# Kernel tuning notes

Measured on AMD Instinct MI355X. Metric: run time of the kernel, lower is better.

The kernel has to match this reference:

```python
import jax, jax.numpy as jnp
import numpy as np

B, T, H, V, L_IN, MAXLEN = 256, 128, 1024, 64, 457, 64


def setup_inputs() -> dict:
    key = jax.random.key(0)
    ks = jax.random.split(key, 12)
    s = 1.0 / np.sqrt(H)  # torch RNN default init scale
    w = lambda k, shape: jax.random.uniform(k, shape, jnp.float32, -s, s)
    z = jnp.zeros((H,), jnp.float32)
    return {
        "x": jax.random.normal(ks[0], (B, T, L_IN), dtype=jnp.float32),
        "emb": w(ks[1], (V, H)),
        # encoder RNN (tanh), 2 layers; b = b_ih + b_hh (mathematically identical)
        "enc_Wih0": w(ks[2], (H, L_IN)), "enc_Whh0": w(ks[3], (H, H)), "enc_b0": z,
        "enc_Wih1": w(ks[4], (H, H)),    "enc_Whh1": w(ks[5], (H, H)), "enc_b1": z,
        # decoder RNN (tanh), 2 layers
        "dec_Wih0": w(ks[6], (H, H)), "dec_Whh0": w(ks[7], (H, H)), "dec_b0": z,
        "dec_Wih1": w(ks[8], (H, H)), "dec_Whh1": w(ks[9], (H, H)), "dec_b1": z,
        "fc_W": w(ks[10], (V, H)), "fc_b": jnp.zeros((V,), jnp.float32),
    }


def _rnn_layer(xs, h0, Wih, Whh, b):
    # xs: [T, B, in]; h_t = tanh(x_t Wih^T + h_{t-1} Whh^T + b)
    def step(h, x_t):
        h = jnp.tanh(x_t @ Wih.T + h @ Whh.T + b)
        return h, h
    h_last, hs = jax.lax.scan(step, h0, xs)
    return hs, h_last


def reference(x, emb, enc_Wih0, enc_Whh0, enc_b0, enc_Wih1, enc_Whh1, enc_b1,
              dec_Wih0, dec_Whh0, dec_b0, dec_Wih1, dec_Whh1, dec_b1, fc_W, fc_b):
    Bc = x.shape[0]
    Hc = enc_Whh0.shape[0]
    xs = jnp.transpose(x, (1, 0, 2))  # [T, B, 457]
    h_init = jnp.zeros((Bc, Hc), x.dtype)
    # encoder: stacked 2-layer vanilla RNN
    hs0, hL0 = _rnn_layer(xs, h_init, enc_Wih0, enc_Whh0, enc_b0)
    hs1, hL1 = _rnn_layer(hs0, h_init, enc_Wih1, enc_Whh1, enc_b1)
    tok0 = jnp.zeros((Bc,), jnp.int32)

    def dec_step(carry, _):
        h0c, h1c, tok = carry
        e = emb[tok]                                        # [B, H]
        h0n = jnp.tanh(e @ dec_Wih0.T + h0c @ dec_Whh0.T + dec_b0)
        h1n = jnp.tanh(h0n @ dec_Wih1.T + h1c @ dec_Whh1.T + dec_b1)
        logits = h1n @ fc_W.T + fc_b                        # [B, V]
        nxt = jnp.argmax(logits, axis=-1).astype(jnp.int32)
        return (h0n, h1n, nxt), logits

    (hd0, hd1, _), logits_seq = jax.lax.scan(dec_step, (hL0, hL1, tok0), None, length=MAXLEN)
    vec_out = jnp.transpose(logits_seq, (1, 2, 0))          # [B, V, maxlen]
    hidden = jnp.stack([hd0, hd1], axis=0)                  # [n_layers, B, H]
    return vec_out, hidden
```

## Files before the change

kernel.cpp:

```cpp
#include <hip/hip_runtime.h>
#include <math.h>


#define Bb   256
#define Tt   128
#define Hh   1024
#define Vv   64
#define LIN  457
#define ML   64
#define NKB_H  32
#define NKB_X  15
#define XST  496

typedef __bf16 bf16;
typedef __bf16 bf16x8 __attribute__((ext_vector_type(8)));
typedef float  f32x4  __attribute__((ext_vector_type(4)));

static __device__ __forceinline__ float bf2f(bf16 x) {
    unsigned short u = __builtin_bit_cast(unsigned short, x);
    unsigned int w = ((unsigned int)u) << 16;
    return __builtin_bit_cast(float, w);
}
static __device__ __forceinline__ unsigned short f2bfbits(float f) {
    unsigned int u = __builtin_bit_cast(unsigned int, f);
    u = u + 0x7FFFu + ((u >> 16) & 1u);
    return (unsigned short)(u >> 16);
}
static __device__ __forceinline__ bf16 f2bf(float f) {
    return __builtin_bit_cast(bf16, f2bfbits(f));
}

#define MFMA(a, b, c) __builtin_amdgcn_mfma_f32_16x16x32_bf16((a), (b), (c), 0, 0, 0)

__global__ __launch_bounds__(256) void pack_w_k(const float* __restrict__ src,
                                                bf16* __restrict__ hp,
                                                bf16* __restrict__ lp,
                                                int nkb, int src_ld, int kmax) {
    const int tid = blockIdx.x * 256 + threadIdx.x;
    const int lane = tid & 63;
    const int kb = (tid >> 6) % nkb;
    const int nt = tid / (64 * nkb);
    if (nt >= 64) return;
    const int row = nt * 16 + (lane & 15);
    const int k0 = kb * 32 + (lane >> 4) * 8;
    const float* s = src + (size_t)row * src_ld;
    bf16x8 h8, l8;
#pragma unroll
    for (int j = 0; j < 8; j++) {
        float v = (k0 + j < kmax) ? s[k0 + j] : 0.f;
        bf16 h = f2bf(v);
        h8[j] = h;
        l8[j] = f2bf(v - bf2f(h));
    }
    *(bf16x8*)(hp + (size_t)tid * 8) = h8;
    *(bf16x8*)(lp + (size_t)tid * 8) = l8;
}

static __device__ __forceinline__ void gemm_pipe(const bf16* __restrict__ ah,
                                                 const bf16* __restrict__ al,
                                                 const bf16* __restrict__ wh,
                                                 const bf16* __restrict__ wl,
                                                 int kb0, int kb1, f32x4* acc) {
    if (kb0 >= kb1) return;
    bf16x8 cah = *(const bf16x8*)(ah + (size_t)kb0 * 512);
    bf16x8 cal = *(const bf16x8*)(al + (size_t)kb0 * 512);
    bf16x8 cwh = *(const bf16x8*)(wh + (size_t)kb0 * 512);
    bf16x8 cwl = *(const bf16x8*)(wl + (size_t)kb0 * 512);
    for (int kb = kb0; kb < kb1; kb++) {
        bf16x8 nah = cah, nal = cal, nwh = cwh, nwl = cwl;
        if (kb + 1 < kb1) {
            nah = *(const bf16x8*)(ah + (size_t)(kb + 1) * 512);
            nal = *(const bf16x8*)(al + (size_t)(kb + 1) * 512);
            nwh = *(const bf16x8*)(wh + (size_t)(kb + 1) * 512);
            nwl = *(const bf16x8*)(wl + (size_t)(kb + 1) * 512);
        }
        *acc = MFMA(cah, cwh, *acc);
        *acc = MFMA(cal, cwh, *acc);
        *acc = MFMA(cah, cwl, *acc);
        cah = nah; cal = nal; cwh = nwh; cwl = nwl;
    }
}

static __device__ __forceinline__ void store_tile(f32x4 acc, int mt, int nt,
                                                  int lm, int quad,
                                                  bf16* __restrict__ ohi,
                                                  bf16* __restrict__ olo) {
    const int o32 = (nt & 1) * 16 + lm;
    const int kbs = nt >> 1;
    const size_t base = (((size_t)mt * 32 + kbs) * 64 + (o32 >> 3) * 16 + quad * 4) * 8
                        + (o32 & 7);
#pragma unroll
    for (int r = 0; r < 4; r++) {
        float h = tanhf(acc[r]);
        bf16 hb = f2bf(h);
        ohi[base + r * 8] = hb;
        olo[base + r * 8] = f2bf(h - bf2f(hb));
    }
}

__global__ __launch_bounds__(256, 2) void enc_step0_k(
    const float* __restrict__ x, int t,
    const bf16* __restrict__ w0h, const bf16* __restrict__ w0l,
    const bf16* __restrict__ hhi, const bf16* __restrict__ hlo,
    const bf16* __restrict__ uh, const bf16* __restrict__ ul,
    const float* __restrict__ bias,
    bf16* __restrict__ ohi, bf16* __restrict__ olo) {
    __shared__ bf16 xh[16 * XST], xl[16 * XST];
    __shared__ float red[2][256];
    const int tid = threadIdx.x;
    const int lane = tid & 63, wave = tid >> 6;
    const int lm = lane & 15, quad = lane >> 4;
    const int tile = wave >> 1, role = wave & 1;
    const int mt = blockIdx.y, nt = blockIdx.x * 2 + tile;
    for (int idx = tid; idx < 16 * XST; idx += 256) {
        int row = idx / XST, col = idx - row * XST;
        float v = (col < LIN) ? x[((size_t)(mt * 16 + row) * Tt + t) * LIN + col] : 0.f;
        bf16 h = f2bf(v);
        xh[idx] = h;
        xl[idx] = f2bf(v - bf2f(h));
    }
    __syncthreads();
    f32x4 acc = (f32x4){0.f, 0.f, 0.f, 0.f};
    const bf16* ah = hhi + ((size_t)mt * 2048 + lane) * 8;
    const bf16* al = hlo + ((size_t)mt * 2048 + lane) * 8;
    const bf16* wha = uh + (size_t)nt * NKB_H * 512 + lane * 8;
    const bf16* wla = ul + (size_t)nt * NKB_H * 512 + lane * 8;
    if (role == 0) {
        float bv = bias[nt * 16 + lm];
        acc = (f32x4){bv, bv, bv, bv};
        const bf16* w0h_ = w0h + (size_t)nt * NKB_X * 512 + lane * 8;
        const bf16* w0l_ = w0l + (size_t)nt * NKB_X * 512 + lane * 8;
        for (int kb = 0; kb < NKB_X; kb++) {
            bf16x8 a1 = *(const bf16x8*)(&xh[lm * XST + kb * 32 + quad * 8]);
            bf16x8 a2 = *(const bf16x8*)(&xl[lm * XST + kb * 32 + quad * 8]);
            bf16x8 wh8 = *(const bf16x8*)(w0h_ + (size_t)kb * 512);
            bf16x8 wl8 = *(const bf16x8*)(w0l_ + (size_t)kb * 512);
            acc = MFMA(a1, wh8, acc);
            acc = MFMA(a2, wh8, acc);
            acc = MFMA(a1, wl8, acc);
        }
        gemm_pipe(ah, al, wha, wla, 0, 9, &acc);
    } else {
        gemm_pipe(ah, al, wha, wla, 9, NKB_H, &acc);
        red[tile][lane * 4 + 0] = acc[0];
        red[tile][lane * 4 + 1] = acc[1];
        red[tile][lane * 4 + 2] = acc[2];
        red[tile][lane * 4 + 3] = acc[3];
    }
    __syncthreads();
    if (role == 0) {
#pragma unroll
        for (int r = 0; r < 4; r++) acc[r] += red[tile][lane * 4 + r];
        store_tile(acc, mt, nt, lm, quad, ohi, olo);
    }
}

__global__ __launch_bounds__(256, 2) void rnn2_step_k(
    const bf16* __restrict__ xhi, const bf16* __restrict__ xlo,
    const bf16* __restrict__ wih, const bf16* __restrict__ wil,
    const bf16* __restrict__ hhi, const bf16* __restrict__ hlo,
    const bf16* __restrict__ whh, const bf16* __restrict__ whl,
    const float* __restrict__ bias,
    bf16* __restrict__ ohi, bf16* __restrict__ olo) {
    __shared__ float red[2][256];
    const int tid = threadIdx.x;
    const int lane = tid & 63, wave = tid >> 6;
    const int lm = lane & 15, quad = lane >> 4;
    const int tile = wave >> 1, role = wave & 1;
    const int mt = blockIdx.y, nt = blockIdx.x * 2 + tile;
    f32x4 acc = (f32x4){0.f, 0.f, 0.f, 0.f};
    if (role == 0) {
        float bv = bias[nt * 16 + lm];
        acc = (f32x4){bv, bv, bv, bv};
        gemm_pipe(xhi + ((size_t)mt * 2048 + lane) * 8,
                  xlo + ((size_t)mt * 2048 + lane) * 8,
                  wih + (size_t)nt * NKB_H * 512 + lane * 8,
                  wil + (size_t)nt * NKB_H * 512 + lane * 8, 0, NKB_H, &acc);
    } else {
        gemm_pipe(hhi + ((size_t)mt * 2048 + lane) * 8,
                  hlo + ((size_t)mt * 2048 + lane) * 8,
                  whh + (size_t)nt * NKB_H * 512 + lane * 8,
                  whl + (size_t)nt * NKB_H * 512 + lane * 8, 0, NKB_H, &acc);
        red[tile][lane * 4 + 0] = acc[0];
        red[tile][lane * 4 + 1] = acc[1];
        red[tile][lane * 4 + 2] = acc[2];
        red[tile][lane * 4 + 3] = acc[3];
    }
    __syncthreads();
    if (role == 0) {
#pragma unroll
        for (int r = 0; r < 4; r++) acc[r] += red[tile][lane * 4 + r];
        store_tile(acc, mt, nt, lm, quad, ohi, olo);
    }
}

__global__ __launch_bounds__(256) void dec_pre_k(const float* __restrict__ emb,
                                                 const float* __restrict__ W,
                                                 const float* __restrict__ b,
                                                 float* __restrict__ EP) {
    const int n = blockIdx.x * 256 + threadIdx.x;
    const int v = blockIdx.y * 4;
    double acc[4];
    const double bv = (double)b[n];
    acc[0] = acc[1] = acc[2] = acc[3] = bv;
    const float* wr = W + (size_t)n * Hh;
#pragma unroll 4
    for (int k = 0; k < Hh; k++) {
        double wv = (double)wr[k];
        acc[0] = fma((double)emb[(size_t)(v + 0) * Hh + k], wv, acc[0]);
        acc[1] = fma((double)emb[(size_t)(v + 1) * Hh + k], wv, acc[1]);
        acc[2] = fma((double)emb[(size_t)(v + 2) * Hh + k], wv, acc[2]);
        acc[3] = fma((double)emb[(size_t)(v + 3) * Hh + k], wv, acc[3]);
    }
#pragma unroll
    for (int r = 0; r < 4; r++) EP[(size_t)(v + r) * Hh + n] = (float)acc[r];
}

__global__ __launch_bounds__(256, 2) void dec_step0_k(
    const float* __restrict__ EP, const int* __restrict__ tok,
    const bf16* __restrict__ hhi, const bf16* __restrict__ hlo,
    const bf16* __restrict__ uh, const bf16* __restrict__ ul,
    bf16* __restrict__ ohi, bf16* __restrict__ olo) {
    __shared__ float red[2][256];
    const int tid = threadIdx.x;
    const int lane = tid & 63, wave = tid >> 6;
    const int lm = lane & 15, quad = lane >> 4;
    const int tile = wave >> 1, role = wave & 1;
    const int mt = blockIdx.y, nt = blockIdx.x * 2 + tile;
    f32x4 acc = (f32x4){0.f, 0.f, 0.f, 0.f};
    const bf16* ah = hhi + ((size_t)mt * 2048 + lane) * 8;
    const bf16* al = hlo + ((size_t)mt * 2048 + lane) * 8;
    const bf16* wha = uh + (size_t)nt * NKB_H * 512 + lane * 8;
    const bf16* wla = ul + (size_t)nt * NKB_H * 512 + lane * 8;
    if (role == 0) {
        gemm_pipe(ah, al, wha, wla, 0, 16, &acc);
    } else {
        gemm_pipe(ah, al, wha, wla, 16, NKB_H, &acc);
        red[tile][lane * 4 + 0] = acc[0];
        red[tile][lane * 4 + 1] = acc[1];
        red[tile][lane * 4 + 2] = acc[2];
        red[tile][lane * 4 + 3] = acc[3];
    }
    __syncthreads();
    if (role == 0) {
        const int n = nt * 16 + lm;
#pragma unroll
        for (int r = 0; r < 4; r++) {
            int tk = tok[mt * 16 + quad * 4 + r];
            acc[r] += red[tile][lane * 4 + r] + EP[(size_t)tk * Hh + n];
        }
        store_tile(acc, mt, nt, lm, quad, ohi, olo);
    }
}

__global__ __launch_bounds__(256) void dec_fc_k(
    const bf16* __restrict__ h1hi, const bf16* __restrict__ h1lo,
    const float* __restrict__ fcw, const float* __restrict__ fcb,
    float* __restrict__ out, int* __restrict__ tok, int t) {
    __shared__ double hrow[4][Hh];
    const int w = threadIdx.x >> 6, v = threadIdx.x & 63;
    const int b = blockIdx.x * 4 + w;
    const int mt = b >> 4, lmb = b & 15;
    for (int k = v; k < Hh; k += 64) {
        size_t idx = (((size_t)mt * 32 + (k >> 5)) * 64 + ((k >> 3) & 3) * 16 + lmb) * 8
                     + (k & 7);
        hrow[w][k] = (double)bf2f(h1hi[idx]) + (double)bf2f(h1lo[idx]);
    }
    __syncthreads();
    const float* wr = fcw + (size_t)v * Hh;
    double a0 = (v == 0) ? 0.0 : 0.0;
    double acc = (double)fcb[v];
#pragma unroll 4
    for (int k = 0; k < Hh; k++) acc = fma(hrow[w][k], (double)wr[k], acc);
    (void)a0;
    out[(size_t)b * (Vv * ML) + (size_t)v * ML + t] = (float)acc;
    double bvv = acc;
    int bi = v;
#pragma unroll
    for (int s = 1; s < 64; s <<= 1) {
        double ov = __shfl_xor(bvv, s, 64);
        int oi = __shfl_xor(bi, s, 64);
        if (ov > bvv || (ov == bvv && oi < bi)) { bvv = ov; bi = oi; }
    }
    if (v == 0) tok[b] = bi;
}

__global__ __launch_bounds__(256) void write_hidden_k(
    const bf16* __restrict__ a1, const bf16* __restrict__ a2,
    const bf16* __restrict__ b1, const bf16* __restrict__ b2,
    float* __restrict__ out) {
    int i = blockIdx.x * 256 + threadIdx.x;
    const int b = i >> 10, k = i & 1023;
    const size_t idx = (((size_t)(b >> 4) * 32 + (k >> 5)) * 64
                        + ((k >> 3) & 3) * 16 + (b & 15)) * 8 + (k & 7);
    const size_t base = (size_t)Bb * Vv * ML;
    out[base + i] = bf2f(a1[idx]) + bf2f(a2[idx]);
    out[base + (size_t)Bb * Hh + i] = bf2f(b1[idx]) + bf2f(b2[idx]);
}

extern "C" void kernel_launch(void* const* d_in, const int* in_sizes, int n_in,
                              void* d_out, int out_size, void* d_ws, size_t ws_size,
                              hipStream_t stream) {
    const float* x   = (const float*)d_in[0];
    const float* emb = (const float*)d_in[1];
    const float* eW0 = (const float*)d_in[2];
    const float* eU0 = (const float*)d_in[3];
    const float* eb0 = (const float*)d_in[4];
    const float* eW1 = (const float*)d_in[5];
    const float* eU1 = (const float*)d_in[6];
    const float* eb1 = (const float*)d_in[7];
    const float* dW0 = (const float*)d_in[8];
    const float* dU0 = (const float*)d_in[9];
    const float* db0 = (const float*)d_in[10];
    const float* dW1 = (const float*)d_in[11];
    const float* dU1 = (const float*)d_in[12];
    const float* db1 = (const float*)d_in[13];
    const float* fcw = (const float*)d_in[14];
    const float* fcb = (const float*)d_in[15];
    (void)in_sizes; (void)n_in; (void)out_size; (void)ws_size;

    char* ws = (char*)d_ws;
    const size_t SB = (size_t)Bb * Hh * 2;
    const size_t WPK = (size_t)64 * NKB_H * 512 * 2;
    const size_t WPX = (size_t)64 * NKB_X * 512 * 2;
    bf16 *h0c[2][2], *h1c[2][2];
    size_t o = 0;
    for (int c = 0; c < 2; c++) { h0c[0][c] = (bf16*)(ws + o); o += SB; }
    for (int c = 0; c < 2; c++) { h1c[0][c] = (bf16*)(ws + o); o += SB; }
    int* tok = (int*)(ws + o); o += 4096;
    const size_t zero_bytes = o;
    for (int c = 0; c < 2; c++) { h0c[1][c] = (bf16*)(ws + o); o += SB; }
    for (int c = 0; c < 2; c++) { h1c[1][c] = (bf16*)(ws + o); o += SB; }
    float* EP = (float*)(ws + o); o += (size_t)Vv * Hh * 4;
    bf16 *w0p[2];
    for (int c = 0; c < 2; c++) { w0p[c] = (bf16*)(ws + o); o += WPX; }
    bf16 *eU0p[2], *eW1p[2], *eU1p[2], *dU0p[2], *dW1p[2], *dU1p[2];
    for (int c = 0; c < 2; c++) { eU0p[c] = (bf16*)(ws + o); o += WPK; }
    for (int c = 0; c < 2; c++) { eW1p[c] = (bf16*)(ws + o); o += WPK; }
    for (int c = 0; c < 2; c++) { eU1p[c] = (bf16*)(ws + o); o += WPK; }
    for (int c = 0; c < 2; c++) { dU0p[c] = (bf16*)(ws + o); o += WPK; }
    for (int c = 0; c < 2; c++) { dW1p[c] = (bf16*)(ws + o); o += WPK; }
    for (int c = 0; c < 2; c++) { dU1p[c] = (bf16*)(ws + o); o += WPK; }

    hipMemsetAsync(ws, 0, zero_bytes, stream);
    dim3 blk(256);
    const int GSQ = 64 * NKB_H * 64 / 256;
    const int GX  = 64 * NKB_X * 64 / 256;
    pack_w_k<<<dim3(GX),  blk, 0, stream>>>(eW0, w0p[0],  w0p[1],  NKB_X, LIN, LIN);
    pack_w_k<<<dim3(GSQ), blk, 0, stream>>>(eU0, eU0p[0], eU0p[1], NKB_H, Hh, Hh);
    pack_w_k<<<dim3(GSQ), blk, 0, stream>>>(eW1, eW1p[0], eW1p[1], NKB_H, Hh, Hh);
    pack_w_k<<<dim3(GSQ), blk, 0, stream>>>(eU1, eU1p[0], eU1p[1], NKB_H, Hh, Hh);
    pack_w_k<<<dim3(GSQ), blk, 0, stream>>>(dU0, dU0p[0], dU0p[1], NKB_H, Hh, Hh);
    pack_w_k<<<dim3(GSQ), blk, 0, stream>>>(dW1, dW1p[0], dW1p[1], NKB_H, Hh, Hh);
    pack_w_k<<<dim3(GSQ), blk, 0, stream>>>(dU1, dU1p[0], dU1p[1], NKB_H, Hh, Hh);

    dim3 g(32, 16);
    float* out = (float*)d_out;
    for (int t = 0; t < Tt; t++) {
        int in = t & 1, op = in ^ 1;
        enc_step0_k<<<g, blk, 0, stream>>>(x, t, w0p[0], w0p[1],
            h0c[in][0], h0c[in][1], eU0p[0], eU0p[1], eb0,
            h0c[op][0], h0c[op][1]);
        rnn2_step_k<<<g, blk, 0, stream>>>(
            h0c[op][0], h0c[op][1], eW1p[0], eW1p[1],
            h1c[in][0], h1c[in][1], eU1p[0], eU1p[1], eb1,
            h1c[op][0], h1c[op][1]);
    }
    dec_pre_k<<<dim3(Hh / 256, Vv / 4), blk, 0, stream>>>(emb, dW0, db0, EP);
    for (int s = 0; s < ML; s++) {
        int in = s & 1, op = in ^ 1;
        dec_step0_k<<<g, blk, 0, stream>>>(EP, tok,
            h0c[in][0], h0c[in][1], dU0p[0], dU0p[1],
            h0c[op][0], h0c[op][1]);
        rnn2_step_k<<<g, blk, 0, stream>>>(
            h0c[op][0], h0c[op][1], dW1p[0], dW1p[1],
            h1c[in][0], h1c[in][1], dU1p[0], dU1p[1], db1,
            h1c[op][0], h1c[op][1]);
        dec_fc_k<<<dim3(Bb / 4), blk, 0, stream>>>(
            h1c[op][0], h1c[op][1], fcw, fcb, out, tok, s);
    }
    write_hidden_k<<<dim3(Bb * Hh / 256), blk, 0, stream>>>(
        h0c[0][0], h0c[0][1], h1c[0][0], h1c[0][1], out);
}
```

Before: 8.541 ms.

## Fuse all RNN timesteps into one persistent cooperative kernel with grid barriers

Replaces the roughly 450 per-step kernel launches for the encoder, decoder and FC/argmax stages with a single cooperative persistent kernel of 256 blocks x 512 threads. Dependent phases are separated by a custom flag-based grid barrier. Each block now handles four output tiles instead of two, and the FC stage splits the K reduction across two waves. This removes launch overhead and inter-kernel gaps, at the cost of spin-wait barrier latency, shared-memory unions that may reduce occupancy, and idle blocks during the FC phase.

```diff
diff --git a/kernel.cpp b/kernel.cpp
--- a/kernel.cpp
+++ b/kernel.cpp
@@ -11,6 +11,8 @@
 #define NKB_H  32
 #define NKB_X  15
 #define XST  496
+#define NBLK 256
+#define NTHR 512
 
 typedef __bf16 bf16;
 typedef __bf16 bf16x8 __attribute__((ext_vector_type(8)));
@@ -98,76 +100,83 @@
     }
 }
 
-__global__ __launch_bounds__(256, 2) void enc_step0_k(
-    const float* __restrict__ x, int t,
-    const bf16* __restrict__ w0h, const bf16* __restrict__ w0l,
-    const bf16* __restrict__ hhi, const bf16* __restrict__ hlo,
-    const bf16* __restrict__ uh, const bf16* __restrict__ ul,
-    const float* __restrict__ bias,
-    bf16* __restrict__ ohi, bf16* __restrict__ olo) {
-    __shared__ bf16 xh[16 * XST], xl[16 * XST];
-    __shared__ float red[2][256];
+__global__ __launch_bounds__(256) void dec_pre_k(const float* __restrict__ emb,
+                                                 const float* __restrict__ W,
+                                                 const float* __restrict__ b,
+                                                 float* __restrict__ EP) {
+    const int n = blockIdx.x * 256 + threadIdx.x;
+    const int v = blockIdx.y * 4;
+    double acc[4];
+    const double bv = (double)b[n];
+    acc[0] = acc[1] = acc[2] = acc[3] = bv;
+    const float* wr = W + (size_t)n * Hh;
+#pragma unroll 4
+    for (int k = 0; k < Hh; k++) {
+        double wv = (double)wr[k];
+        acc[0] = fma((double)emb[(size_t)(v + 0) * Hh + k], wv, acc[0]);
+        acc[1] = fma((double)emb[(size_t)(v + 1) * Hh + k], wv, acc[1]);
+        acc[2] = fma((double)emb[(size_t)(v + 2) * Hh + k], wv, acc[2]);
+        acc[3] = fma((double)emb[(size_t)(v + 3) * Hh + k], wv, acc[3]);
+    }
+#pragma unroll
+    for (int r = 0; r < 4; r++) EP[(size_t)(v + r) * Hh + n] = (float)acc[r];
+}
+
+struct Params {
+    const float* x;
+    const bf16 *w0h, *w0l;
+    const bf16 *eU0h, *eU0l, *eW1h, *eW1l, *eU1h, *eU1l;
+    const bf16 *dU0h, *dU0l, *dW1h, *dW1l, *dU1h, *dU1l;
+    const float *eb0, *eb1, *db1;
+    const float *EP, *fcw, *fcb;
+    float* out;
+    int* tok;
+    bf16* h0[2][2];
+    bf16* h1[2][2];
+    unsigned* flags;
+    unsigned* gen;
+};
+
+static __device__ __forceinline__ void gbar(unsigned* flags, unsigned* gen,
+                                            unsigned ph) {
+    __syncthreads();
     const int tid = threadIdx.x;
-    const int lane = tid & 63, wave = tid >> 6;
-    const int lm = lane & 15, quad = lane >> 4;
-    const int tile = wave >> 1, role = wave & 1;
-    const int mt = blockIdx.y, nt = blockIdx.x * 2 + tile;
-    for (int idx = tid; idx < 16 * XST; idx += 256) {
-        int row = idx / XST, col = idx - row * XST;
-        float v = (col < LIN) ? x[((size_t)(mt * 16 + row) * Tt + t) * LIN + col] : 0.f;
-        bf16 h = f2bf(v);
-        xh[idx] = h;
-        xl[idx] = f2bf(v - bf2f(h));
+    if (blockIdx.x == 0) {
+        if (tid > 0 && tid < NBLK) {
+            while (__hip_atomic_load(flags + tid, __ATOMIC_RELAXED,
+                                     __HIP_MEMORY_SCOPE_AGENT) < ph)
+                __builtin_amdgcn_s_sleep(1);
+        }
+        __syncthreads();
+        if (tid == 0) {
+            __hip_atomic_store(gen, ph, __ATOMIC_RELEASE,
+                               __HIP_MEMORY_SCOPE_AGENT);
+            (void)__hip_atomic_load(gen, __ATOMIC_ACQUIRE,
+                                    __HIP_MEMORY_SCOPE_AGENT);
+        }
+    } else {
+        if (tid == 0) {
+            __hip_atomic_store(flags + blockIdx.x, ph, __ATOMIC_RELEASE,
+                               __HIP_MEMORY_SCOPE_AGENT);
+            while (__hip_atomic_load(gen, __ATOMIC_RELAXED,
+                                     __HIP_MEMORY_SCOPE_AGENT) < ph)
+                __builtin_amdgcn_s_sleep(1);
+            (void)__hip_atomic_load(gen, __ATOMIC_ACQUIRE,
+                                    __HIP_MEMORY_SCOPE_AGENT);
+        }
     }
     __syncthreads();
-    f32x4 acc = (f32x4){0.f, 0.f, 0.f, 0.f};
-    const bf16* ah = hhi + ((size_t)mt * 2048 + lane) * 8;
-    const bf16* al = hlo + ((size_t)mt * 2048 + lane) * 8;
-    const bf16* wha = uh + (size_t)nt * NKB_H * 512 + lane * 8;
-    const bf16* wla = ul + (size_t)nt * NKB_H * 512 + lane * 8;
-    if (role == 0) {
-        float bv = bias[nt * 16 + lm];
-        acc = (f32x4){bv, bv, bv, bv};
-        const bf16* w0h_ = w0h + (size_t)nt * NKB_X * 512 + lane * 8;
-        const bf16* w0l_ = w0l + (size_t)nt * NKB_X * 512 + lane * 8;
-        for (int kb = 0; kb < NKB_X; kb++) {
-            bf16x8 a1 = *(const bf16x8*)(&xh[lm * XST + kb * 32 + quad * 8]);
-            bf16x8 a2 = *(const bf16x8*)(&xl[lm * XST + kb * 32 + quad * 8]);
-            bf16x8 wh8 = *(const bf16x8*)(w0h_ + (size_t)kb * 512);
-            bf16x8 wl8 = *(const bf16x8*)(w0l_ + (size_t)kb * 512);
-            acc = MFMA(a1, wh8, acc);
-            acc = MFMA(a2, wh8, acc);
-            acc = MFMA(a1, wl8, acc);
-        }
-        gemm_pipe(ah, al, wha, wla, 0, 9, &acc);
-    } else {
-        gemm_pipe(ah, al, wha, wla, 9, NKB_H, &acc);
-        red[tile][lane * 4 + 0] = acc[0];
-        red[tile][lane * 4 + 1] = acc[1];
-        red[tile][lane * 4 + 2] = acc[2];
-        red[tile][lane * 4 + 3] = acc[3];
-    }
-    __syncthreads();
-    if (role == 0) {
-#pragma unroll
-        for (int r = 0; r < 4; r++) acc[r] += red[tile][lane * 4 + r];
-        store_tile(acc, mt, nt, lm, quad, ohi, olo);
-    }
-}
-
-__global__ __launch_bounds__(256, 2) void rnn2_step_k(
+}
+
+static __device__ __forceinline__ void phase_rnn2(
     const bf16* __restrict__ xhi, const bf16* __restrict__ xlo,
     const bf16* __restrict__ wih, const bf16* __restrict__ wil,
     const bf16* __restrict__ hhi, const bf16* __restrict__ hlo,
     const bf16* __restrict__ whh, const bf16* __restrict__ whl,
     const float* __restrict__ bias,
-    bf16* __restrict__ ohi, bf16* __restrict__ olo) {
-    __shared__ float red[2][256];
-    const int tid = threadIdx.x;
-    const int lane = tid & 63, wave = tid >> 6;
-    const int lm = lane & 15, quad = lane >> 4;
-    const int tile = wave >> 1, role = wave & 1;
-    const int mt = blockIdx.y, nt = blockIdx.x * 2 + tile;
+    bf16* __restrict__ ohi, bf16* __restrict__ olo,
+    int mt, int nt, int tile, int role, int lane, int lm, int quad,
+    float (*red)[256]) {
     f32x4 acc = (f32x4){0.f, 0.f, 0.f, 0.f};
     if (role == 0) {
         float bv = bias[nt * 16 + lm];
@@ -194,108 +203,167 @@
     }
 }
 
-__global__ __launch_bounds__(256) void dec_pre_k(const float* __restrict__ emb,
-                                                 const float* __restrict__ W,
-                                                 const float* __restrict__ b,
-                                                 float* __restrict__ EP) {
-    const int n = blockIdx.x * 256 + threadIdx.x;
-    const int v = blockIdx.y * 4;
-    double acc[4];
-    const double bv = (double)b[n];
-    acc[0] = acc[1] = acc[2] = acc[3] = bv;
-    const float* wr = W + (size_t)n * Hh;
-#pragma unroll 4
-    for (int k = 0; k < Hh; k++) {
-        double wv = (double)wr[k];
-        acc[0] = fma((double)emb[(size_t)(v + 0) * Hh + k], wv, acc[0]);
-        acc[1] = fma((double)emb[(size_t)(v + 1) * Hh + k], wv, acc[1]);
-        acc[2] = fma((double)emb[(size_t)(v + 2) * Hh + k], wv, acc[2]);
-        acc[3] = fma((double)emb[(size_t)(v + 3) * Hh + k], wv, acc[3]);
-    }
-#pragma unroll
-    for (int r = 0; r < 4; r++) EP[(size_t)(v + r) * Hh + n] = (float)acc[r];
-}
-
-__global__ __launch_bounds__(256, 2) void dec_step0_k(
-    const float* __restrict__ EP, const int* __restrict__ tok,
-    const bf16* __restrict__ hhi, const bf16* __restrict__ hlo,
-    const bf16* __restrict__ uh, const bf16* __restrict__ ul,
-    bf16* __restrict__ ohi, bf16* __restrict__ olo) {
-    __shared__ float red[2][256];
+__global__ __launch_bounds__(NTHR, 2) void persist_k(Params p) {
+    __shared__ union {
+        struct { bf16 xh[16 * XST]; bf16 xl[16 * XST]; } xs;
+        double hrow[4][Hh];
+    } su;
+    __shared__ union {
+        float red[4][256];
+        double dred[4][64];
+    } ru;
+
     const int tid = threadIdx.x;
+    const int blk = blockIdx.x;
     const int lane = tid & 63, wave = tid >> 6;
     const int lm = lane & 15, quad = lane >> 4;
     const int tile = wave >> 1, role = wave & 1;
-    const int mt = blockIdx.y, nt = blockIdx.x * 2 + tile;
-    f32x4 acc = (f32x4){0.f, 0.f, 0.f, 0.f};
-    const bf16* ah = hhi + ((size_t)mt * 2048 + lane) * 8;
-    const bf16* al = hlo + ((size_t)mt * 2048 + lane) * 8;
-    const bf16* wha = uh + (size_t)nt * NKB_H * 512 + lane * 8;
-    const bf16* wla = ul + (size_t)nt * NKB_H * 512 + lane * 8;
-    if (role == 0) {
-        gemm_pipe(ah, al, wha, wla, 0, 16, &acc);
-    } else {
-        gemm_pipe(ah, al, wha, wla, 16, NKB_H, &acc);
-        red[tile][lane * 4 + 0] = acc[0];
-        red[tile][lane * 4 + 1] = acc[1];
-        red[tile][lane * 4 + 2] = acc[2];
-        red[tile][lane * 4 + 3] = acc[3];
-    }
-    __syncthreads();
-    if (role == 0) {
-        const int n = nt * 16 + lm;
-#pragma unroll
-        for (int r = 0; r < 4; r++) {
-            int tk = tok[mt * 16 + quad * 4 + r];
-            acc[r] += red[tile][lane * 4 + r] + EP[(size_t)tk * Hh + n];
-        }
-        store_tile(acc, mt, nt, lm, quad, ohi, olo);
-    }
-}
-
-__global__ __launch_bounds__(256) void dec_fc_k(
-    const bf16* __restrict__ h1hi, const bf16* __restrict__ h1lo,
-    const float* __restrict__ fcw, const float* __restrict__ fcb,
-    float* __restrict__ out, int* __restrict__ tok, int t) {
-    __shared__ double hrow[4][Hh];
-    const int w = threadIdx.x >> 6, v = threadIdx.x & 63;
-    const int b = blockIdx.x * 4 + w;
-    const int mt = b >> 4, lmb = b & 15;
-    for (int k = v; k < Hh; k += 64) {
-        size_t idx = (((size_t)mt * 32 + (k >> 5)) * 64 + ((k >> 3) & 3) * 16 + lmb) * 8
-                     + (k & 7);
-        hrow[w][k] = (double)bf2f(h1hi[idx]) + (double)bf2f(h1lo[idx]);
-    }
-    __syncthreads();
-    const float* wr = fcw + (size_t)v * Hh;
-    double a0 = (v == 0) ? 0.0 : 0.0;
-    double acc = (double)fcb[v];
-#pragma unroll 4
-    for (int k = 0; k < Hh; k++) acc = fma(hrow[w][k], (double)wr[k], acc);
-    (void)a0;
-    out[(size_t)b * (Vv * ML) + (size_t)v * ML + t] = (float)acc;
-    double bvv = acc;
-    int bi = v;
-#pragma unroll
-    for (int s = 1; s < 64; s <<= 1) {
-        double ov = __shfl_xor(bvv, s, 64);
-        int oi = __shfl_xor(bi, s, 64);
-        if (ov > bvv || (ov == bvv && oi < bi)) { bvv = ov; bi = oi; }
-    }
-    if (v == 0) tok[b] = bi;
-}
-
-__global__ __launch_bounds__(256) void write_hidden_k(
-    const bf16* __restrict__ a1, const bf16* __restrict__ a2,
-    const bf16* __restrict__ b1, const bf16* __restrict__ b2,
-    float* __restrict__ out) {
-    int i = blockIdx.x * 256 + threadIdx.x;
-    const int b = i >> 10, k = i & 1023;
-    const size_t idx = (((size_t)(b >> 4) * 32 + (k >> 5)) * 64
-                        + ((k >> 3) & 3) * 16 + (b & 15)) * 8 + (k & 7);
-    const size_t base = (size_t)Bb * Vv * ML;
-    out[base + i] = bf2f(a1[idx]) + bf2f(a2[idx]);
-    out[base + (size_t)Bb * Hh + i] = bf2f(b1[idx]) + bf2f(b2[idx]);
+    const int mt = blk >> 4;
+    const int nt = (blk & 15) * 4 + tile;
+    unsigned ph = 0;
+
+    for (int t = 0; t < Tt; t++) {
+        const int in = t & 1, op = in ^ 1;
+        {
+            for (int idx = tid; idx < 16 * XST; idx += NTHR) {
+                int row = idx / XST, col = idx - row * XST;
+                float v = (col < LIN)
+                    ? p.x[((size_t)(mt * 16 + row) * Tt + t) * LIN + col] : 0.f;
+                bf16 h = f2bf(v);
+                su.xs.xh[idx] = h;
+                su.xs.xl[idx] = f2bf(v - bf2f(h));
+            }
+            __syncthreads();
+            f32x4 acc = (f32x4){0.f, 0.f, 0.f, 0.f};
+            const bf16* ah = p.h0[in][0] + ((size_t)mt * 2048 + lane) * 8;
+            const bf16* al = p.h0[in][1] + ((size_t)mt * 2048 + lane) * 8;
+            const bf16* wha = p.eU0h + (size_t)nt * NKB_H * 512 + lane * 8;
+            const bf16* wla = p.eU0l + (size_t)nt * NKB_H * 512 + lane * 8;
+            if (role == 0) {
+                float bv = p.eb0[nt * 16 + lm];
+                acc = (f32x4){bv, bv, bv, bv};
+                const bf16* w0h_ = p.w0h + (size_t)nt * NKB_X * 512 + lane * 8;
+                const bf16* w0l_ = p.w0l + (size_t)nt * NKB_X * 512 + lane * 8;
+                for (int kb = 0; kb < NKB_X; kb++) {
+                    bf16x8 a1 = *(const bf16x8*)(&su.xs.xh[lm * XST + kb * 32 + quad * 8]);
+                    bf16x8 a2 = *(const bf16x8*)(&su.xs.xl[lm * XST + kb * 32 + quad * 8]);
+                    bf16x8 wh8 = *(const bf16x8*)(w0h_ + (size_t)kb * 512);
+                    bf16x8 wl8 = *(const bf16x8*)(w0l_ + (size_t)kb * 512);
+                    acc = MFMA(a1, wh8, acc);
+                    acc = MFMA(a2, wh8, acc);
+                    acc = MFMA(a1, wl8, acc);
+                }
+                gemm_pipe(ah, al, wha, wla, 0, 9, &acc);
+            } else {
+                gemm_pipe(ah, al, wha, wla, 9, NKB_H, &acc);
+                ru.red[tile][lane * 4 + 0] = acc[0];
+                ru.red[tile][lane * 4 + 1] = acc[1];
+                ru.red[tile][lane * 4 + 2] = acc[2];
+                ru.red[tile][lane * 4 + 3] = acc[3];
+            }
+            __syncthreads();
+            if (role == 0) {
+#pragma unroll
+                for (int r = 0; r < 4; r++) acc[r] += ru.red[tile][lane * 4 + r];
+                store_tile(acc, mt, nt, lm, quad, p.h0[op][0], p.h0[op][1]);
+            }
+        }
+        gbar(p.flags, p.gen, ++ph);
+        phase_rnn2(p.h0[op][0], p.h0[op][1], p.eW1h, p.eW1l,
+                   p.h1[in][0], p.h1[in][1], p.eU1h, p.eU1l, p.eb1,
+                   p.h1[op][0], p.h1[op][1],
+                   mt, nt, tile, role, lane, lm, quad, ru.red);
+        gbar(p.flags, p.gen, ++ph);
+    }
+
+    for (int s = 0; s < ML; s++) {
+        const int in = s & 1, op = in ^ 1;
+        {
+            f32x4 acc = (f32x4){0.f, 0.f, 0.f, 0.f};
+            const bf16* ah = p.h0[in][0] + ((size_t)mt * 2048 + lane) * 8;
+            const bf16* al = p.h0[in][1] + ((size_t)mt * 2048 + lane) * 8;
+            const bf16* wha = p.dU0h + (size_t)nt * NKB_H * 512 + lane * 8;
+            const bf16* wla = p.dU0l + (size_t)nt * NKB_H * 512 + lane * 8;
+            if (role == 0) {
+                gemm_pipe(ah, al, wha, wla, 0, 16, &acc);
+            } else {
+                gemm_pipe(ah, al, wha, wla, 16, NKB_H, &acc);
+                ru.red[tile][lane * 4 + 0] = acc[0];
+                ru.red[tile][lane * 4 + 1] = acc[1];
+                ru.red[tile][lane * 4 + 2] = acc[2];
+                ru.red[tile][lane * 4 + 3] = acc[3];
+            }
+            __syncthreads();
+            if (role == 0) {
+                const int n = nt * 16 + lm;
+#pragma unroll
+                for (int r = 0; r < 4; r++) {
+                    int tk = p.tok[mt * 16 + quad * 4 + r];
+                    acc[r] += ru.red[tile][lane * 4 + r] + p.EP[(size_t)tk * Hh + n];
+                }
+                store_tile(acc, mt, nt, lm, quad, p.h0[op][0], p.h0[op][1]);
+            }
+        }
+        gbar(p.flags, p.gen, ++ph);
+        phase_rnn2(p.h0[op][0], p.h0[op][1], p.dW1h, p.dW1l,
+                   p.h1[in][0], p.h1[in][1], p.dU1h, p.dU1l, p.db1,
+                   p.h1[op][0], p.h1[op][1],
+                   mt, nt, tile, role, lane, lm, quad, ru.red);
+        gbar(p.flags, p.gen, ++ph);
+        if (blk < 64) {
+            const bf16* h1hi = p.h1[op][0];
+            const bf16* h1lo = p.h1[op][1];
+            for (int i = tid; i < 4 * Hh; i += NTHR) {
+                int r = i >> 10, k = i & 1023;
+                int b = blk * 4 + r;
+                size_t id = (((size_t)(b >> 4) * 32 + (k >> 5)) * 64
+                             + ((k >> 3) & 3) * 16 + (b & 15)) * 8 + (k & 7);
+                su.hrow[r][k] = (double)bf2f(h1hi[id]) + (double)bf2f(h1lo[id]);
+            }
+            __syncthreads();
+            const int r = wave >> 1, half = wave & 1;
+            const int v = lane;
+            const int b = blk * 4 + r;
+            const float* wr = p.fcw + (size_t)v * Hh;
+            double a0 = 0.0, a1 = 0.0, a2 = 0.0, a3 = 0.0;
+            const int k0 = half * 512;
+            for (int k = k0; k < k0 + 512; k += 4) {
+                a0 = fma(su.hrow[r][k + 0], (double)wr[k + 0], a0);
+                a1 = fma(su.hrow[r][k + 1], (double)wr[k + 1], a1);
+                a2 = fma(su.hrow[r][k + 2], (double)wr[k + 2], a2);
+                a3 = fma(su.hrow[r][k + 3], (double)wr[k + 3], a3);
+            }
+            double part = (a0 + a1) + (a2 + a3);
+            if (half == 1) ru.dred[r][v] = part;
+            __syncthreads();
+            if (half == 0) {
+                double acc = part + ru.dred[r][v] + (double)p.fcb[v];
+                p.out[(size_t)b * (Vv * ML) + (size_t)v * ML + s] = (float)acc;
+                double bvv = acc;
+                int bi = v;
+#pragma unroll
+                for (int st = 1; st < 64; st <<= 1) {
+                    double ov = __shfl_xor(bvv, st, 64);
+                    int oi = __shfl_xor(bi, st, 64);
+                    if (ov > bvv || (ov == bvv && oi < bi)) { bvv = ov; bi = oi; }
+                }
+                if (v == 0) p.tok[b] = bi;
+            }
+        }
+        gbar(p.flags, p.gen, ++ph);
+    }
+
+    {
+        const size_t base = (size_t)Bb * Vv * ML;
+        for (int i = blk * NTHR + tid; i < Bb * Hh; i += NBLK * NTHR) {
+            const int b = i >> 10, k = i & 1023;
+            const size_t idx = (((size_t)(b >> 4) * 32 + (k >> 5)) * 64
+                                + ((k >> 3) & 3) * 16 + (b & 15)) * 8 + (k & 7);
+            p.out[base + i] = bf2f(p.h0[0][0][idx]) + bf2f(p.h0[0][1][idx]);
+            p.out[base + (size_t)Bb * Hh + i] =
+                bf2f(p.h1[0][0][idx]) + bf2f(p.h1[0][1][idx]);
+        }
+    }
 }
 
 extern "C" void kernel_launch(void* const* d_in, const int* in_sizes, int n_in,
@@ -327,7 +395,9 @@
     size_t o = 0;
     for (int c = 0; c < 2; c++) { h0c[0][c] = (bf16*)(ws + o); o += SB; }
     for (int c = 0; c < 2; c++) { h1c[0][c] = (bf16*)(ws + o); o += SB; }
-    int* tok = (int*)(ws + o); o += 4096;
+    int* tok = (int*)(ws + o); o += 1024;
+    unsigned* flags = (unsigned*)(ws + o); o += NBLK * 4;
+    unsigned* gen = (unsigned*)(ws + o); o += 256;
     const size_t zero_bytes = o;
     for (int c = 0; c < 2; c++) { h0c[1][c] = (bf16*)(ws + o); o += SB; }
     for (int c = 0; c < 2; c++) { h1c[1][c] = (bf16*)(ws + o); o += SB; }
@@ -353,32 +423,29 @@
     pack_w_k<<<dim3(GSQ), blk, 0, stream>>>(dU0, dU0p[0], dU0p[1], NKB_H, Hh, Hh);
     pack_w_k<<<dim3(GSQ), blk, 0, stream>>>(dW1, dW1p[0], dW1p[1], NKB_H, Hh, Hh);
     pack_w_k<<<dim3(GSQ), blk, 0, stream>>>(dU1, dU1p[0], dU1p[1], NKB_H, Hh, Hh);
-
-    dim3 g(32, 16);
-    float* out = (float*)d_out;
-    for (int t = 0; t < Tt; t++) {
-        int in = t & 1, op = in ^ 1;
-        enc_step0_k<<<g, blk, 0, stream>>>(x, t, w0p[0], w0p[1],
-            h0c[in][0], h0c[in][1], eU0p[0], eU0p[1], eb0,
-            h0c[op][0], h0c[op][1]);
-        rnn2_step_k<<<g, blk, 0, stream>>>(
-            h0c[op][0], h0c[op][1], eW1p[0], eW1p[1],
-            h1c[in][0], h1c[in][1], eU1p[0], eU1p[1], eb1,
-            h1c[op][0], h1c[op][1]);
-    }
     dec_pre_k<<<dim3(Hh / 256, Vv / 4), blk, 0, stream>>>(emb, dW0, db0, EP);
-    for (int s = 0; s < ML; s++) {
-        int in = s & 1, op = in ^ 1;
-        dec_step0_k<<<g, blk, 0, stream>>>(EP, tok,
-            h0c[in][0], h0c[in][1], dU0p[0], dU0p[1],
-            h0c[op][0], h0c[op][1]);
-        rnn2_step_k<<<g, blk, 0, stream>>>(
-            h0c[op][0], h0c[op][1], dW1p[0], dW1p[1],
-            h1c[in][0], h1c[in][1], dU1p[0], dU1p[1], db1,
-            h1c[op][0], h1c[op][1]);
-        dec_fc_k<<<dim3(Bb / 4), blk, 0, stream>>>(
-            h1c[op][0], h1c[op][1], fcw, fcb, out, tok, s);
-    }
-    write_hidden_k<<<dim3(Bb * Hh / 256), blk, 0, stream>>>(
-        h0c[0][0], h0c[0][1], h1c[0][0], h1c[0][1], out);
-}
+
+    Params pr;
+    pr.x = x;
+    pr.w0h = w0p[0];  pr.w0l = w0p[1];
+    pr.eU0h = eU0p[0]; pr.eU0l = eU0p[1];
+    pr.eW1h = eW1p[0]; pr.eW1l = eW1p[1];
+    pr.eU1h = eU1p[0]; pr.eU1l = eU1p[1];
+    pr.dU0h = dU0p[0]; pr.dU0l = dU0p[1];
+    pr.dW1h = dW1p[0]; pr.dW1l = dW1p[1];
+    pr.dU1h = dU1p[0]; pr.dU1l = dU1p[1];
+    pr.eb0 = eb0; pr.eb1 = eb1; pr.db1 = db1;
+    pr.EP = EP; pr.fcw = fcw; pr.fcb = fcb;
+    pr.out = (float*)d_out;
+    pr.tok = tok;
+    for (int pp = 0; pp < 2; pp++)
+        for (int c = 0; c < 2; c++) {
+            pr.h0[pp][c] = h0c[pp][c];
+            pr.h1[pp][c] = h1c[pp][c];
+        }
+    pr.flags = flags; pr.gen = gen;
+
+    void* kargs[] = { (void*)&pr };
+    hipLaunchCooperativeKernel((void*)persist_k, dim3(NBLK), dim3(NTHR),
+                               kargs, 0, stream);
+}
```

New measurement: 13.40 ms. 56.9% more time.
